# Kernel tuning notes

Hardware: AMD Instinct MI355X
Metric: run time of the kernel (lower is better)

## Reference

```python
import jax, jax.numpy as jnp
import numpy as np


def setup_inputs() -> dict:
    key = jax.random.key(0)
    k1, k2, k3 = jax.random.split(key, 3)
    B, H, HKV, S, D = 2, 32, 8, 2048, 128
    q = jax.random.normal(k1, (B, H, S, D), dtype=jnp.float32)
    k = jax.random.normal(k2, (B, HKV, S, D), dtype=jnp.float32)
    v = jax.random.normal(k3, (B, HKV, S, D), dtype=jnp.float32)
    return {"q": q, "k": k, "v": v}


def reference(q, k, v):
    # GQA: query head j attends with KV head j // num_groups (repeat_interleave
    # semantics). Instead of materializing repeated K/V, reshape Q into
    # [B, Hkv, G, S, D] and contract against shared KV heads directly.
    B, H, S, D = q.shape
    Hkv = k.shape[1]
    G = H // Hkv
    qg = q.reshape(B, Hkv, G, S, D)
    scale = 1.0 / jnp.sqrt(jnp.asarray(D, q.dtype))
    # scores: [B, Hkv, G, Sq, Sk]
    scores = jnp.einsum('bhgqd,bhkd->bhgqk', qg, k) * scale
    # is_causal=True: lower-triangular mask
    causal = jnp.tril(jnp.ones((S, S), dtype=bool))
    scores = jnp.where(causal, scores, jnp.finfo(scores.dtype).min)
    attn = jax.nn.softmax(scores, axis=-1)
    out = jnp.einsum('bhgqk,bhkd->bhgqd', attn, v)
    return out.reshape(B, H, S, D)
```

## Files before the change

kernel.cpp:

```cpp
#include <hip/hip_runtime.h>
#include <hip/hip_bf16.h>
#include <cstdint>

typedef __bf16 bf16;
typedef __bf16 bf16x8 __attribute__((ext_vector_type(8)));
typedef float f32x4 __attribute__((ext_vector_type(4)));
typedef unsigned int u32;
typedef __attribute__((address_space(3))) uint32_t lds_u32;
typedef const __attribute__((address_space(1))) uint32_t glb_u32;

#define B_ 2
#define H_ 32
#define HKV_ 8
#define S_ 2048
#define D_ 128
#define QT 128
#define KT 64
#define NQT (S_ / QT)
#define NTILES (S_ / KT)
#define TILE_ELEMS (KT * D_)
#define NEG_BIG (-1.0e30f)
#define SCL 0.12751745f
#define DEFER_THR 8.0f

__device__ __forceinline__ bf16x8 cvt8p(float4 a, float4 b) {
  bf16x8 r = {(bf16)a.x, (bf16)a.y, (bf16)a.z, (bf16)a.w,
              (bf16)b.x, (bf16)b.y, (bf16)b.z, (bf16)b.w};
  return r;
}
__device__ __forceinline__ bf16x8 cvt8(const float* f) {
  return cvt8p(*(const float4*)f, *(const float4*)(f + 4));
}
__device__ __forceinline__ u32 pk2(float lo, float hi) {
  union { bf16 h[2]; u32 w; } u;
  u.h[0] = (bf16)lo; u.h[1] = (bf16)hi;
  return u.w;
}

__global__ __launch_bounds__(512) void prep(const float* __restrict__ k,
                                            const float* __restrict__ v,
                                            bf16* __restrict__ kws,
                                            bf16* __restrict__ vws) {
  __shared__ float Vf[KT * 129];
  const int blk = blockIdx.x;
  const int bhkv = blk >> 5, tile = blk & 31;
  const float* ks = k + ((size_t)bhkv * S_ + (size_t)tile * KT) * D_;
  const float* vs = v + ((size_t)bhkv * S_ + (size_t)tile * KT) * D_;
  bf16* kd = kws + (size_t)blk * TILE_ELEMS;
  bf16* vd = vws + (size_t)blk * TILE_ELEMS;
  const int t = threadIdx.x;
#pragma unroll
  for (int i = 0; i < 4; ++i) {
    int c = t + 512 * i, row = c >> 5, c4 = c & 31;
    *(float4*)&Vf[row * 129 + c4 * 4] = *(const float4*)(vs + row * D_ + c4 * 4);
  }
#pragma unroll
  for (int i = 0; i < 2; ++i) {
    int chunk = t + 512 * i, row = chunk >> 4, c16 = chunk & 15;
    int e = (c16 ^ (row & 7)) << 3;
    *(bf16x8*)&kd[chunk * 8] = cvt8(ks + row * D_ + e);
  }
  __syncthreads();
#pragma unroll
  for (int i = 0; i < 2; ++i) {
    int chunk = t + 512 * i, d = chunk >> 3, c8 = chunk & 7;
    int k0 = (c8 ^ (d & 7)) << 3;
    bf16x8 val;
#pragma unroll
    for (int kk = 0; kk < 8; ++kk) val[kk] = (bf16)Vf[(k0 + kk) * 129 + d];
    *(bf16x8*)&vd[chunk * 8] = val;
  }
}

__global__ __launch_bounds__(512, 4) void fa_mfma(
    const float* __restrict__ q, const bf16* __restrict__ kws,
    const bf16* __restrict__ vws, float* __restrict__ out) {
  __shared__ bf16 Kb2[2][TILE_ELEMS];
  __shared__ bf16 Vb[TILE_ELEMS];

  const int tid = threadIdx.x, wave = tid >> 6, lane = tid & 63;
  const int col = lane & 15, quad = lane >> 4;
  const int bid = blockIdx.x;
  const int tqt = (NQT - 1) - (bid >> 6);
  const int bh = bid & 63, b = bh >> 5, h = bh & 31, hkv = h >> 2;
  const int bhkv = b * HKV_ + hkv;

  const float* qh = q + (size_t)(b * H_ + h) * S_ * D_;
  float* oh = out + (size_t)(b * H_ + h) * S_ * D_;
  const bf16* kg = kws + (size_t)(bhkv * NTILES) * TILE_ELEMS;
  const bf16* vg = vws + (size_t)(bhkv * NTILES) * TILE_ELEMS;
  const int q0 = tqt * QT;
  const int jmax = 2 * tqt + 1;

  bf16x8 qf[4];
  {
    const float* qrow = qh + (size_t)(q0 + wave * 16 + col) * D_ + quad * 8;
#pragma unroll
    for (int ks = 0; ks < 4; ++ks) qf[ks] = cvt8(qrow + ks * 32);
  }

  f32x4 o[8];
#pragma unroll
  for (int i = 0; i < 8; ++i) o[i] = (f32x4){0.f, 0.f, 0.f, 0.f};
  float m_i = NEG_BIG, lp = 0.f;

  const int qoff = (quad * 16) ^ ((col & 7) << 4);
  const int qx[4] = {qoff, qoff ^ 64, qoff ^ 128, qoff ^ 192};

  const int stoff = tid * 16;

  auto stageK = [&](int j, int buf) {
    const char* src = (const char*)(kg + (size_t)j * TILE_ELEMS) + stoff;
    char* dst = (char*)Kb2[buf] + stoff;
#pragma unroll
    for (int i = 0; i < 2; ++i)
      __builtin_amdgcn_global_load_lds((glb_u32*)(src + i * 8192),
                                       (lds_u32*)(dst + i * 8192), 16, 0, 0);
  };
  auto stageV = [&](int j) {
    const char* src = (const char*)(vg + (size_t)j * TILE_ELEMS) + stoff;
    char* dst = (char*)Vb + stoff;
#pragma unroll
    for (int i = 0; i < 2; ++i)
      __builtin_amdgcn_global_load_lds((glb_u32*)(src + i * 8192),
                                       (lds_u32*)(dst + i * 8192), 16, 0, 0);
  };

  stageK(0, 0);
  asm volatile("s_waitcnt vmcnt(0)" ::: "memory");
  __builtin_amdgcn_s_barrier();
  __builtin_amdgcn_sched_barrier(0);

  for (int j = 0; j <= jmax; ++j) {
    const int cur = j & 1;
    stageV(j);
    if (j < jmax) stageK(j + 1, cur ^ 1);

    const char* Kb = (const char*)Kb2[cur];

    float s[4][4];
    __builtin_amdgcn_s_setprio(1);
#pragma unroll
    for (int nt = 0; nt < 4; ++nt) {
      const char* An = Kb + (nt * 16 + col) * 256;
      f32x4 acc = (f32x4){0.f, 0.f, 0.f, 0.f};
#pragma unroll
      for (int ks = 0; ks < 4; ++ks) {
        bf16x8 kf = *(const bf16x8*)(An + qx[ks]);
        acc = __builtin_amdgcn_mfma_f32_16x16x32_bf16(kf, qf[ks], acc, 0, 0, 0);
      }
#pragma unroll
      for (int r = 0; r < 4; ++r) s[nt][r] = acc[r] * SCL;
    }
    __builtin_amdgcn_s_setprio(0);

    if (j >= 2 * tqt) {
      const int rel = j * KT - q0 - wave * 16;
#pragma unroll
      for (int nt = 0; nt < 4; ++nt)
#pragma unroll
        for (int r = 0; r < 4; ++r)
          if (rel + nt * 16 + quad * 4 + r > col) s[nt][r] = NEG_BIG;
    }

    float mx = s[0][0];
#pragma unroll
    for (int nt = 0; nt < 4; ++nt)
#pragma unroll
      for (int r = 0; r < 4; ++r) mx = fmaxf(mx, s[nt][r]);
    mx = fmaxf(mx, __shfl_xor(mx, 16, 64));
    mx = fmaxf(mx, __shfl_xor(mx, 32, 64));

    if (__any(mx - m_i > DEFER_THR)) {
      float mnew = fmaxf(m_i, mx);
      float alpha = exp2f(m_i - mnew);
      lp *= alpha;
      m_i = mnew;
#pragma unroll
      for (int dt = 0; dt < 8; ++dt) o[dt] *= alpha;
    }

    float rs = 0.f;
#pragma unroll
    for (int nt = 0; nt < 4; ++nt)
#pragma unroll
      for (int r = 0; r < 4; ++r) {
        s[nt][r] = exp2f(s[nt][r] - m_i);
        rs += s[nt][r];
      }
    lp += rs;

    u32 pk_[4][2];
#pragma unroll
    for (int nt = 0; nt < 4; ++nt) {
      pk_[nt][0] = pk2(s[nt][0], s[nt][1]);
      pk_[nt][1] = pk2(s[nt][2], s[nt][3]);
    }
    const bool oddq = (quad & 1);
    union W8 { u32 w[4]; bf16x8 h; } pf[2];
#pragma unroll
    for (int ks = 0; ks < 2; ++ks)
#pragma unroll
      for (int p = 0; p < 2; ++p) {
        auto sw = __builtin_amdgcn_permlane32_swap(pk_[2 * ks][p],
                                                   pk_[2 * ks + 1][p],
                                                   false, false);
        u32 Qp = (u32)sw[0], Rp = (u32)sw[1];
        u32 Tp = (u32)__shfl_xor((int)Qp, 16, 64);
        u32 Sp = (u32)__shfl_xor((int)Rp, 16, 64);
        pf[ks].w[p] = oddq ? Sp : Qp;
        pf[ks].w[2 + p] = oddq ? Rp : Tp;
      }

    if (j < jmax)
      asm volatile("s_waitcnt vmcnt(2)" ::: "memory");
    else
      asm volatile("s_waitcnt vmcnt(0)" ::: "memory");
    __builtin_amdgcn_s_barrier();
    __builtin_amdgcn_sched_barrier(0);

    __builtin_amdgcn_s_setprio(1);
#pragma unroll
    for (int dt = 0; dt < 8; ++dt) {
      const char* Av = (const char*)Vb + (dt * 16 + col) * 128;
#pragma unroll
      for (int ks = 0; ks < 2; ++ks) {
        bf16x8 vf = *(const bf16x8*)(Av + qx[ks]);
        o[dt] = __builtin_amdgcn_mfma_f32_16x16x32_bf16(vf, pf[ks].h, o[dt], 0, 0, 0);
      }
    }
    __builtin_amdgcn_s_setprio(0);

    if (j < jmax) {
      asm volatile("s_waitcnt vmcnt(0)" ::: "memory");
      __builtin_amdgcn_s_barrier();
      __builtin_amdgcn_sched_barrier(0);
    }
  }

  float l = lp;
  l += __shfl_xor(l, 16, 64);
  l += __shfl_xor(l, 32, 64);
  const float inv = 1.f / l;
  float* orow = oh + (size_t)(q0 + wave * 16 + col) * D_;
#pragma unroll
  for (int dt = 0; dt < 8; ++dt) {
    f32x4 vout = o[dt] * inv;
    *(f32x4*)&orow[dt * 16 + quad * 4] = vout;
  }
}

extern "C" void kernel_launch(void* const* d_in, const int* in_sizes, int n_in,
                              void* d_out, int out_size, void* d_ws, size_t ws_size,
                              hipStream_t stream) {
  const int QN = B_ * H_ * S_ * D_;
  int qi, ki, vi;
  if (in_sizes[0] == QN)      { qi = 0; ki = 1; vi = 2; }
  else if (in_sizes[1] == QN) { qi = 1; ki = 0; vi = 2; }
  else                        { qi = 2; ki = 0; vi = 1; }
  const float* q = (const float*)d_in[qi];
  const float* k = (const float*)d_in[ki];
  const float* v = (const float*)d_in[vi];
  float* out = (float*)d_out;

  bf16* kws = (bf16*)d_ws;
  bf16* vws = kws + (size_t)(B_ * HKV_) * NTILES * TILE_ELEMS;

  prep<<<dim3(B_ * HKV_ * NTILES), dim3(512), 0, stream>>>(k, v, kws, vws);
  fa_mfma<<<dim3(B_ * H_ * NQT), dim3(512), 0, stream>>>(q, kws, vws, out);
}
```

Measured before the change: 241.1 us.

## Double KV tile to 128 rows with single-buffered K/V staging and prescaled Q

Raises the key tile from 64 to 128 rows, so each loop iteration runs twice as many MFMAs and half as many barriers and softmax bookkeeping steps. K and V each use one 32KB LDS buffer instead of double-buffered K. The next K load is issued after the QK MFMAs finish, and the next V load after the PV stage. The softmax scale is folded into Q when it is converted to bf16, which removes a multiply per score. The trade-offs are more register pressure from s[8][4] and pf[4], and less overlap between loads and compute, since the next tile only starts loading after the current one has been consumed.

```diff
diff --git a/kernel.cpp b/kernel.cpp
--- a/kernel.cpp
+++ b/kernel.cpp
@@ -15,10 +15,10 @@
 #define S_ 2048
 #define D_ 128
 #define QT 128
-#define KT 64
+#define KT 128
 #define NQT (S_ / QT)
-#define NTILES (S_ / KT)
-#define TILE_ELEMS (KT * D_)
+#define NIMG (S_ / 64)
+#define IMG_ELEMS (64 * D_)
 #define NEG_BIG (-1.0e30f)
 #define SCL 0.12751745f
 #define DEFER_THR 8.0f
@@ -31,6 +31,12 @@
 __device__ __forceinline__ bf16x8 cvt8(const float* f) {
   return cvt8p(*(const float4*)f, *(const float4*)(f + 4));
 }
+__device__ __forceinline__ bf16x8 cvt8s(const float* f, float s) {
+  float4 a = *(const float4*)f, b = *(const float4*)(f + 4);
+  bf16x8 r = {(bf16)(a.x * s), (bf16)(a.y * s), (bf16)(a.z * s), (bf16)(a.w * s),
+              (bf16)(b.x * s), (bf16)(b.y * s), (bf16)(b.z * s), (bf16)(b.w * s)};
+  return r;
+}
 __device__ __forceinline__ u32 pk2(float lo, float hi) {
   union { bf16 h[2]; u32 w; } u;
   u.h[0] = (bf16)lo; u.h[1] = (bf16)hi;
@@ -41,13 +47,13 @@
                                             const float* __restrict__ v,
                                             bf16* __restrict__ kws,
                                             bf16* __restrict__ vws) {
-  __shared__ float Vf[KT * 129];
+  __shared__ float Vf[64 * 129];
   const int blk = blockIdx.x;
-  const int bhkv = blk >> 5, tile = blk & 31;
-  const float* ks = k + ((size_t)bhkv * S_ + (size_t)tile * KT) * D_;
-  const float* vs = v + ((size_t)bhkv * S_ + (size_t)tile * KT) * D_;
-  bf16* kd = kws + (size_t)blk * TILE_ELEMS;
-  bf16* vd = vws + (size_t)blk * TILE_ELEMS;
+  const int bhkv = blk >> 5, img = blk & 31;
+  const float* ks = k + ((size_t)bhkv * S_ + (size_t)img * 64) * D_;
+  const float* vs = v + ((size_t)bhkv * S_ + (size_t)img * 64) * D_;
+  bf16* kd = kws + (size_t)blk * IMG_ELEMS;
+  bf16* vd = vws + (size_t)blk * IMG_ELEMS;
   const int t = threadIdx.x;
 #pragma unroll
   for (int i = 0; i < 4; ++i) {
@@ -75,8 +81,8 @@
 __global__ __launch_bounds__(512, 4) void fa_mfma(
     const float* __restrict__ q, const bf16* __restrict__ kws,
     const bf16* __restrict__ vws, float* __restrict__ out) {
-  __shared__ bf16 Kb2[2][TILE_ELEMS];
-  __shared__ bf16 Vb[TILE_ELEMS];
+  __shared__ bf16 Kb[2 * IMG_ELEMS];
+  __shared__ bf16 Vb[2 * IMG_ELEMS];
 
   const int tid = threadIdx.x, wave = tid >> 6, lane = tid & 63;
   const int col = lane & 15, quad = lane >> 4;
@@ -87,16 +93,16 @@
 
   const float* qh = q + (size_t)(b * H_ + h) * S_ * D_;
   float* oh = out + (size_t)(b * H_ + h) * S_ * D_;
-  const bf16* kg = kws + (size_t)(bhkv * NTILES) * TILE_ELEMS;
-  const bf16* vg = vws + (size_t)(bhkv * NTILES) * TILE_ELEMS;
+  const bf16* kg = kws + (size_t)(bhkv * NIMG) * IMG_ELEMS;
+  const bf16* vg = vws + (size_t)(bhkv * NIMG) * IMG_ELEMS;
   const int q0 = tqt * QT;
-  const int jmax = 2 * tqt + 1;
+  const int jmax = tqt;
 
   bf16x8 qf[4];
   {
     const float* qrow = qh + (size_t)(q0 + wave * 16 + col) * D_ + quad * 8;
 #pragma unroll
-    for (int ks = 0; ks < 4; ++ks) qf[ks] = cvt8(qrow + ks * 32);
+    for (int ks = 0; ks < 4; ++ks) qf[ks] = cvt8s(qrow + ks * 32, SCL);
   }
 
   f32x4 o[8];
@@ -109,40 +115,35 @@
 
   const int stoff = tid * 16;
 
-  auto stageK = [&](int j, int buf) {
-    const char* src = (const char*)(kg + (size_t)j * TILE_ELEMS) + stoff;
-    char* dst = (char*)Kb2[buf] + stoff;
-#pragma unroll
-    for (int i = 0; i < 2; ++i)
+  auto stageK = [&](int j) {
+    const char* src = (const char*)kg + (size_t)j * 32768 + stoff;
+    char* dst = (char*)Kb + stoff;
+#pragma unroll
+    for (int i = 0; i < 4; ++i)
       __builtin_amdgcn_global_load_lds((glb_u32*)(src + i * 8192),
                                        (lds_u32*)(dst + i * 8192), 16, 0, 0);
   };
   auto stageV = [&](int j) {
-    const char* src = (const char*)(vg + (size_t)j * TILE_ELEMS) + stoff;
+    const char* src = (const char*)vg + (size_t)j * 32768 + stoff;
     char* dst = (char*)Vb + stoff;
 #pragma unroll
-    for (int i = 0; i < 2; ++i)
+    for (int i = 0; i < 4; ++i)
       __builtin_amdgcn_global_load_lds((glb_u32*)(src + i * 8192),
                                        (lds_u32*)(dst + i * 8192), 16, 0, 0);
   };
 
-  stageK(0, 0);
+  stageK(0);
+  stageV(0);
   asm volatile("s_waitcnt vmcnt(0)" ::: "memory");
   __builtin_amdgcn_s_barrier();
   __builtin_amdgcn_sched_barrier(0);
 
   for (int j = 0; j <= jmax; ++j) {
-    const int cur = j & 1;
-    stageV(j);
-    if (j < jmax) stageK(j + 1, cur ^ 1);
-
-    const char* Kb = (const char*)Kb2[cur];
-
-    float s[4][4];
+    float s[8][4];
     __builtin_amdgcn_s_setprio(1);
 #pragma unroll
-    for (int nt = 0; nt < 4; ++nt) {
-      const char* An = Kb + (nt * 16 + col) * 256;
+    for (int nt = 0; nt < 8; ++nt) {
+      const char* An = (const char*)Kb + (nt * 16 + col) * 256;
       f32x4 acc = (f32x4){0.f, 0.f, 0.f, 0.f};
 #pragma unroll
       for (int ks = 0; ks < 4; ++ks) {
@@ -150,24 +151,29 @@
         acc = __builtin_amdgcn_mfma_f32_16x16x32_bf16(kf, qf[ks], acc, 0, 0, 0);
       }
 #pragma unroll
-      for (int r = 0; r < 4; ++r) s[nt][r] = acc[r] * SCL;
+      for (int r = 0; r < 4; ++r) s[nt][r] = acc[r];
     }
     __builtin_amdgcn_s_setprio(0);
 
-    if (j >= 2 * tqt) {
-      const int rel = j * KT - q0 - wave * 16;
-#pragma unroll
-      for (int nt = 0; nt < 4; ++nt)
+    __builtin_amdgcn_s_barrier();
+    __builtin_amdgcn_sched_barrier(0);
+    if (j < jmax) stageK(j + 1);
+
+    if (j == tqt) {
+      const int rowq = wave * 16 + col;
+#pragma unroll
+      for (int nt = 0; nt < 8; ++nt)
 #pragma unroll
         for (int r = 0; r < 4; ++r)
-          if (rel + nt * 16 + quad * 4 + r > col) s[nt][r] = NEG_BIG;
-    }
-
-    float mx = s[0][0];
-#pragma unroll
-    for (int nt = 0; nt < 4; ++nt)
-#pragma unroll
-      for (int r = 0; r < 4; ++r) mx = fmaxf(mx, s[nt][r]);
+          if (nt * 16 + quad * 4 + r > rowq) s[nt][r] = NEG_BIG;
+    }
+
+    float m4[8];
+#pragma unroll
+    for (int nt = 0; nt < 8; ++nt)
+      m4[nt] = fmaxf(fmaxf(s[nt][0], s[nt][1]), fmaxf(s[nt][2], s[nt][3]));
+    float mx = fmaxf(fmaxf(fmaxf(m4[0], m4[1]), fmaxf(m4[2], m4[3])),
+                     fmaxf(fmaxf(m4[4], m4[5]), fmaxf(m4[6], m4[7])));
     mx = fmaxf(mx, __shfl_xor(mx, 16, 64));
     mx = fmaxf(mx, __shfl_xor(mx, 32, 64));
 
@@ -182,7 +188,7 @@
 
     float rs = 0.f;
 #pragma unroll
-    for (int nt = 0; nt < 4; ++nt)
+    for (int nt = 0; nt < 8; ++nt)
 #pragma unroll
       for (int r = 0; r < 4; ++r) {
         s[nt][r] = exp2f(s[nt][r] - m_i);
@@ -190,16 +196,16 @@
       }
     lp += rs;
 
-    u32 pk_[4][2];
-#pragma unroll
-    for (int nt = 0; nt < 4; ++nt) {
+    u32 pk_[8][2];
+#pragma unroll
+    for (int nt = 0; nt < 8; ++nt) {
       pk_[nt][0] = pk2(s[nt][0], s[nt][1]);
       pk_[nt][1] = pk2(s[nt][2], s[nt][3]);
     }
     const bool oddq = (quad & 1);
-    union W8 { u32 w[4]; bf16x8 h; } pf[2];
-#pragma unroll
-    for (int ks = 0; ks < 2; ++ks)
+    union W8 { u32 w[4]; bf16x8 h; } pf[4];
+#pragma unroll
+    for (int ks = 0; ks < 4; ++ks)
 #pragma unroll
       for (int p = 0; p < 2; ++p) {
         auto sw = __builtin_amdgcn_permlane32_swap(pk_[2 * ks][p],
@@ -213,7 +219,7 @@
       }
 
     if (j < jmax)
-      asm volatile("s_waitcnt vmcnt(2)" ::: "memory");
+      asm volatile("s_waitcnt vmcnt(4)" ::: "memory");
     else
       asm volatile("s_waitcnt vmcnt(0)" ::: "memory");
     __builtin_amdgcn_s_barrier();
@@ -222,10 +228,11 @@
     __builtin_amdgcn_s_setprio(1);
 #pragma unroll
     for (int dt = 0; dt < 8; ++dt) {
-      const char* Av = (const char*)Vb + (dt * 16 + col) * 128;
-#pragma unroll
-      for (int ks = 0; ks < 2; ++ks) {
-        bf16x8 vf = *(const bf16x8*)(Av + qx[ks]);
+#pragma unroll
+      for (int ks = 0; ks < 4; ++ks) {
+        const char* Av = (const char*)Vb + (ks >> 1) * 16384 +
+                         (dt * 16 + col) * 128 + (qoff ^ ((ks & 1) << 6));
+        bf16x8 vf = *(const bf16x8*)Av;
         o[dt] = __builtin_amdgcn_mfma_f32_16x16x32_bf16(vf, pf[ks].h, o[dt], 0, 0, 0);
       }
     }
@@ -235,6 +242,7 @@
       asm volatile("s_waitcnt vmcnt(0)" ::: "memory");
       __builtin_amdgcn_s_barrier();
       __builtin_amdgcn_sched_barrier(0);
+      stageV(j + 1);
     }
   }
 
@@ -264,8 +272,8 @@
   float* out = (float*)d_out;
 
   bf16* kws = (bf16*)d_ws;
-  bf16* vws = kws + (size_t)(B_ * HKV_) * NTILES * TILE_ELEMS;
-
-  prep<<<dim3(B_ * HKV_ * NTILES), dim3(512), 0, stream>>>(k, v, kws, vws);
+  bf16* vws = kws + (size_t)(B_ * HKV_) * NIMG * IMG_ELEMS;
+
+  prep<<<dim3(B_ * HKV_ * NIMG), dim3(512), 0, stream>>>(k, v, kws, vws);
   fa_mfma<<<dim3(B_ * H_ * NQT), dim3(512), 0, stream>>>(q, kws, vws, out);
 }
```

After: 239.3 us. Within noise of the previous version (-0.8%).
